# Kernel tuning notes

Measured on AMD Instinct MI355X. Metric: run time of the kernel, lower is better.

## Reference

```python
import jax, jax.numpy as jnp
import numpy as np

# tag2index constants
PAD, START, END, T = 0, 14, 15, 16
B, L, V, E, H = 128, 512, 30000, 256, 256


def _lstm(xs, w_ih, w_hh, b, reverse=False):
    """xs: [L, B, E] -> hs: [L, B, H]. PyTorch gate order i,f,g,o."""
    Bsz = xs.shape[1]
    Hd = w_hh.shape[1]
    def cell(carry, xt):
        h, c = carry
        g = xt @ w_ih.T + h @ w_hh.T + b  # [B, 4H]
        i, f, gg, o = jnp.split(g, 4, axis=-1)
        c = jax.nn.sigmoid(f) * c + jax.nn.sigmoid(i) * jnp.tanh(gg)
        h = jax.nn.sigmoid(o) * jnp.tanh(c)
        return (h, c), h
    init = (jnp.zeros((Bsz, Hd), xs.dtype), jnp.zeros((Bsz, Hd), xs.dtype))
    _, hs = jax.lax.scan(cell, init, xs, reverse=reverse)
    return hs


def setup_inputs() -> dict:
    key = jax.random.key(0)
    ks = jax.random.split(key, 12)
    batch_data = jax.random.randint(ks[0], (B, L), 0, V, dtype=jnp.int32)
    # variable-length tags with contiguous trailing PAD (as the model assumes)
    lengths = jax.random.randint(ks[1], (B,), L // 4, L + 1)
    raw_tags = jax.random.randint(ks[2], (B, L), 1, 14, dtype=jnp.int32)  # real tags in [1,14)
    pos = jnp.arange(L)[None, :]
    batch_tag = jnp.where(pos < lengths[:, None], raw_tags, PAD).astype(jnp.int32)
    s = 0.05
    emb = jax.random.normal(ks[3], (V, E), jnp.float32) * s
    w_ih_f = jax.random.normal(ks[4], (4 * H, E), jnp.float32) * s
    w_hh_f = jax.random.normal(ks[5], (4 * H, H), jnp.float32) * s
    b_f = jnp.zeros((4 * H,), jnp.float32)
    w_ih_b = jax.random.normal(ks[6], (4 * H, E), jnp.float32) * s
    w_hh_b = jax.random.normal(ks[7], (4 * H, H), jnp.float32) * s
    b_b = jnp.zeros((4 * H,), jnp.float32)
    w_cls = jax.random.normal(ks[8], (T, 2 * H), jnp.float32) * s
    b_cls = jnp.zeros((T,), jnp.float32)
    transition = jnp.full((T, T), 1.0 / T, jnp.float32)
    return {"batch_data": batch_data, "batch_tag": batch_tag, "emb": emb,
            "w_ih_f": w_ih_f, "w_hh_f": w_hh_f, "b_f": b_f,
            "w_ih_b": w_ih_b, "w_hh_b": w_hh_b, "b_b": b_b,
            "w_cls": w_cls, "b_cls": b_cls, "transition": transition}


def reference(batch_data, batch_tag, emb, w_ih_f, w_hh_f, b_f,
              w_ih_b, w_hh_b, b_b, w_cls, b_cls, transition):
    # ---- BiLSTM encoder ----
    x = emb[batch_data]                      # [B, L, E]
    xs = jnp.moveaxis(x, 1, 0)               # [L, B, E]
    hf = _lstm(xs, w_ih_f, w_hh_f, b_f, reverse=False)
    hb = _lstm(xs, w_ih_b, w_hh_b, b_b, reverse=True)
    out = jnp.moveaxis(jnp.concatenate([hf, hb], axis=-1), 0, 1)  # [B, L, 2H]
    emission = out @ w_cls.T + b_cls          # [B, L, T]
    crf_scores = emission[:, :, None, :] + transition[None, None]  # [B, L, T, T]

    # ---- CRF loss (linear-chain forward algorithm) ----
    mask = batch_tag != PAD                   # [B, L]
    lengths = mask.sum(axis=1)                # [B]
    prev = jnp.concatenate(
        [jnp.full((B, 1), START, batch_tag.dtype), batch_tag[:, :-1]], axis=1)
    idx = (batch_tag + prev * T).astype(jnp.int32)  # flat (prev_tag, cur_tag) index
    flat = crf_scores.reshape(B, L, T * T)
    g = jnp.take_along_axis(flat, idx[:, :, None], axis=2)[..., 0]
    golden_scores = jnp.sum(jnp.where(mask, g, 0.0))

    sc_t = jnp.moveaxis(crf_scores, 1, 0)     # [L, B, T, T]
    init = sc_t[0, :, START, :]               # [B, T] (all lengths >= 1)
    def step(prev_scores, x_t):
        sc, t = x_t
        new = jax.nn.logsumexp(sc + prev_scores[:, :, None], axis=1)  # [B, T]
        active = (lengths > t)[:, None]
        return jnp.where(active, new, prev_scores), None
    final, _ = jax.lax.scan(step, init, (sc_t[1:], jnp.arange(1, L)))
    all_path_scores = jnp.sum(final[:, END])
    loss = (all_path_scores - golden_scores) / B
    return loss
```

## Files before the change

kernel.cpp:

```cpp
#include <hip/hip_runtime.h>

#define Bsz 128
#define Lseq 512
#define Hdim 256
#define Tn 16
#define START_TAG 14
#define END_TAG 15

typedef float f32x4 __attribute__((ext_vector_type(4)));
typedef short s16x8 __attribute__((ext_vector_type(8)));

__device__ __forceinline__ unsigned short f2bf(float f) {
    unsigned int u = __builtin_bit_cast(unsigned int, f);
    u += 0x7fffu + ((u >> 16) & 1u);
    return (unsigned short)(u >> 16);
}
__device__ __forceinline__ float bf2f(unsigned int bits16) {
    return __builtin_bit_cast(float, bits16 << 16);
}
__device__ __forceinline__ float sigmoidf_(float x) {
    return 1.0f / (1.0f + __expf(-x));
}

__global__ void embprep_kernel(const float* __restrict__ emb,
                               unsigned int* __restrict__ embb, int n2) {
    int i = blockIdx.x * blockDim.x + threadIdx.x;
    int stride = gridDim.x * blockDim.x;
    for (; i < n2; i += stride)
        embb[i] = (unsigned int)f2bf(emb[2 * i]) | ((unsigned int)f2bf(emb[2 * i + 1]) << 16);
}

__global__ void wprep_kernel(const float* __restrict__ wih_f, const float* __restrict__ whh_f,
                             const float* __restrict__ wih_b, const float* __restrict__ whh_b,
                             unsigned int* __restrict__ wtile) {
    int bid = blockIdx.x;
    int ki  = bid & 15;
    int tl  = (bid >> 4) & 3;
    int ug  = (bid >> 6) & 15;
    int dir = bid >> 10;
    int t = threadIdx.x;
    int lane = t >> 2, j = t & 3;
    int n = lane & 15, kq = lane >> 4;
    int k0 = ki * 32 + kq * 8 + 2 * j;
    int col = tl * 256 + ug * 16 + n;
    const float* wih = dir ? wih_b : wih_f;
    const float* whh = dir ? whh_b : whh_f;
    float f0, f1;
    if (k0 < 256) { f0 = wih[col * 256 + k0];       f1 = wih[col * 256 + k0 + 1]; }
    else          { f0 = whh[col * 256 + k0 - 256]; f1 = whh[col * 256 + k0 - 255]; }
    wtile[(size_t)bid * 256 + t] = (unsigned int)f2bf(f0) | ((unsigned int)f2bf(f1) << 16);
}

__global__ void lengths_kernel(const int* __restrict__ tag, int* __restrict__ lengths) {
    int b = blockIdx.x;
    int tid = threadIdx.x;
    int cnt = 0;
    for (int l = tid; l < Lseq; l += blockDim.x)
        cnt += (tag[b * Lseq + l] != 0) ? 1 : 0;
    for (int off = 32; off > 0; off >>= 1) cnt += __shfl_down(cnt, off);
    __shared__ int red[4];
    if ((tid & 63) == 0) red[tid >> 6] = cnt;
    __syncthreads();
    if (tid == 0) lengths[b] = red[0] + red[1] + red[2] + red[3];
}

__global__ __launch_bounds__(256, 1) void bilstm_persist(
    const int* __restrict__ bd,
    const unsigned int* __restrict__ embb,
    const unsigned int* __restrict__ wtile,
    const float* __restrict__ b_f, const float* __restrict__ b_b,
    const float* __restrict__ w_cls,
    float* __restrict__ em_f, float* __restrict__ em_b,
    unsigned long long* __restrict__ ring)
{
    const int wg  = blockIdx.x;
    const int dir = wg >> 7;
    const int bg  = (wg >> 4) & 7;
    const int ug  = wg & 15;
    const int tid = threadIdx.x;
    const int gb0 = bg * 16;

    __shared__ unsigned int w_lds[16384];
    __shared__ unsigned int h_lds[16 * 132];
    __shared__ float g_lds[4][16][17];
    __shared__ float part_lds[16][17];
    __shared__ float bias_lds[64];
    __shared__ float wcls_lds[256];

    {
        const unsigned int* wsrc = wtile + ((size_t)(dir * 16 + ug) << 14);
        for (int i = 0; i < 16; ++i) {
            int idx = tid + 256 * i;
            uint4 v4 = *(const uint4*)(wsrc + (size_t)idx * 4);
            *(uint4*)&w_lds[idx * 4] = v4;
        }
        if (tid < 64) {
            const float* bias = dir ? b_b : b_f;
            bias_lds[tid] = bias[(tid >> 4) * 256 + ug * 16 + (tid & 15)];
        }
        wcls_lds[tid] = w_cls[(size_t)ug * (2 * Hdim) + dir * Hdim + tid];
        for (int i = tid; i < 16 * 132; i += 256) h_lds[i] = 0;
    }

    const int wv = tid >> 6;
    const int l  = tid & 63;
    const int n  = l & 15;
    const int kq = l >> 4;
    const int cb = tid >> 4, cu = tid & 15;
    const int em_m = tid >> 4, em_seg = tid & 15;
    const int hm = tid >> 4, hj0 = (tid & 15) * 8;
    float c_reg = 0.f;
    float* emout = dir ? em_b : em_f;
    const int* bd_row = bd + (size_t)(gb0 + n) * Lseq;

    unsigned long long* rbase = ring + (size_t)dir * 2 * 16384;

    __syncthreads();

    f32x4 acc_x = {0.f, 0.f, 0.f, 0.f};
    {
        const int t0 = dir ? (Lseq - 1) : 0;
        int tok = bd_row[t0];
        const unsigned int* xsrc = embb + (size_t)tok * 128 + kq * 4;
        #pragma unroll
        for (int ki = 0; ki < 8; ++ki) {
            uint4 xv = *(const uint4*)(xsrc + ki * 16);
            s16x8 a = __builtin_bit_cast(s16x8, xv);
            s16x8 b = *(const s16x8*)&w_lds[((wv * 16 + ki) * 64 + l) * 4];
            acc_x = __builtin_amdgcn_mfma_f32_16x16x32_bf16(a, b, acc_x, 0, 0, 0);
        }
    }
    int tok_next = (Lseq > 1) ? bd_row[dir ? (Lseq - 2) : 1] : 0;

    unsigned long long v[8];

    for (int s = 0; s < Lseq; ++s) {
        if (s > 0) {
            #pragma unroll
            for (int j = 0; j < 8; ++j)
                h_lds[hm * 132 + hj0 + j] = (unsigned int)v[j];
        }
        __syncthreads();

        if (s > 0) {
            const unsigned int* hr = &h_lds[em_m * 132 + em_seg * 8];
            const float* wc = &wcls_lds[em_seg * 16];
            float p = 0.f;
            #pragma unroll
            for (int j = 0; j < 8; ++j) {
                unsigned int w = hr[j];
                p += bf2f(w & 0xffffu) * wc[2 * j] + bf2f(w >> 16) * wc[2 * j + 1];
            }
            part_lds[em_m][em_seg] = p;
        }
        {
            f32x4 acc = acc_x;
            #pragma unroll
            for (int kih = 0; kih < 8; ++kih) {
                s16x8 a = *(const s16x8*)&h_lds[n * 132 + kih * 16 + kq * 4];
                s16x8 b = *(const s16x8*)&w_lds[(((wv * 16) + 8 + kih) * 64 + l) * 4];
                acc = __builtin_amdgcn_mfma_f32_16x16x32_bf16(a, b, acc, 0, 0, 0);
            }
            #pragma unroll
            for (int r = 0; r < 4; ++r)
                g_lds[wv][kq * 4 + r][n] = acc[r];
        }
        __syncthreads();

        {
            float gi = g_lds[0][cb][cu] + bias_lds[cu];
            float gf = g_lds[1][cb][cu] + bias_lds[16 + cu];
            float gg = g_lds[2][cb][cu] + bias_lds[32 + cu];
            float go = g_lds[3][cb][cu] + bias_lds[48 + cu];
            float cn = sigmoidf_(gf) * c_reg + sigmoidf_(gi) * tanhf(gg);
            c_reg = cn;
            float hn = sigmoidf_(go) * tanhf(cn);
            unsigned int hbits = (unsigned int)f2bf(hn);
            unsigned int other = (unsigned int)__shfl_down((int)hbits, 1);
            if ((cu & 1) == 0) {
                unsigned long long pk = (unsigned long long)(hbits | (other << 16))
                                      | ((unsigned long long)(s + 1) << 32);
                __hip_atomic_store(
                    rbase + ((size_t)(s & 1) * 16384) + (size_t)(gb0 + cb) * 128 + ug * 8 + (cu >> 1),
                    pk, __ATOMIC_RELAXED, __HIP_MEMORY_SCOPE_AGENT);
            }
        }

        if (s + 1 < Lseq) {
            const unsigned int* xsrc = embb + (size_t)tok_next * 128 + kq * 4;
            f32x4 ax = {0.f, 0.f, 0.f, 0.f};
            #pragma unroll
            for (int ki = 0; ki < 8; ++ki) {
                uint4 xv = *(const uint4*)(xsrc + ki * 16);
                s16x8 a = __builtin_bit_cast(s16x8, xv);
                s16x8 b = *(const s16x8*)&w_lds[((wv * 16 + ki) * 64 + l) * 4];
                ax = __builtin_amdgcn_mfma_f32_16x16x32_bf16(a, b, ax, 0, 0, 0);
            }
            acc_x = ax;
        }
        if (s + 2 < Lseq)
            tok_next = bd_row[dir ? (Lseq - 3 - s) : (s + 2)];

        const unsigned long long* src =
            rbase + ((size_t)(s & 1) * 16384) + (size_t)(gb0 + hm) * 128 + hj0;
        #pragma unroll
        for (int j = 0; j < 8; ++j)
            v[j] = __hip_atomic_load(src + j, __ATOMIC_RELAXED, __HIP_MEMORY_SCOPE_AGENT);

        if (s > 0 && tid < 16) {
            float ssum = 0.f;
            #pragma unroll
            for (int q = 0; q < 16; ++q) ssum += part_lds[tid][q];
            int t_prev = dir ? (Lseq - s) : (s - 1);
            emout[((size_t)(gb0 + tid) * Lseq + t_prev) * Tn + ug] = ssum;
        }

        {
            const unsigned long long want = (unsigned long long)(s + 1);
            unsigned int pend = 0xffu;
            int tries = 0;
            while (true) {
                #pragma unroll
                for (int j = 0; j < 8; ++j)
                    if ((pend & (1u << j)) && ((v[j] >> 32) == want))
                        pend &= ~(1u << j);
                if (!pend) break;
                if (tries++ > 0) __builtin_amdgcn_s_sleep(2);
                #pragma unroll
                for (int j = 0; j < 8; ++j)
                    if (pend & (1u << j))
                        v[j] = __hip_atomic_load(src + j, __ATOMIC_RELAXED,
                                                 __HIP_MEMORY_SCOPE_AGENT);
            }
        }
    }

    {
        #pragma unroll
        for (int j = 0; j < 8; ++j)
            h_lds[hm * 132 + hj0 + j] = (unsigned int)v[j];
        __syncthreads();
        {
            const unsigned int* hr = &h_lds[em_m * 132 + em_seg * 8];
            const float* wc = &wcls_lds[em_seg * 16];
            float p = 0.f;
            #pragma unroll
            for (int j = 0; j < 8; ++j) {
                unsigned int vv = hr[j];
                p += bf2f(vv & 0xffffu) * wc[2 * j] + bf2f(vv >> 16) * wc[2 * j + 1];
            }
            part_lds[em_m][em_seg] = p;
        }
        __syncthreads();
        if (tid < 16) {
            float ssum = 0.f;
            #pragma unroll
            for (int q = 0; q < 16; ++q) ssum += part_lds[tid][q];
            int t_tail = dir ? 0 : (Lseq - 1);
            emout[((size_t)(gb0 + tid) * Lseq + t_tail) * Tn + ug] = ssum;
        }
    }
}

__global__ void golden_kernel(const int* __restrict__ tag,
                              const float* __restrict__ em_f,
                              const float* __restrict__ em_b,
                              const float* __restrict__ b_cls,
                              const float* __restrict__ trans,
                              float* __restrict__ golden)
{
    int b = blockIdx.x;
    int tid = threadIdx.x;
    float s = 0.f;
    for (int l = tid; l < Lseq; l += blockDim.x) {
        int tg = tag[b * Lseq + l];
        if (tg != 0) {
            int prev = (l == 0) ? START_TAG : tag[b * Lseq + l - 1];
            size_t e = ((size_t)b * Lseq + l) * Tn + tg;
            s += em_f[e] + em_b[e] + b_cls[tg] + trans[prev * Tn + tg];
        }
    }
    for (int off = 32; off > 0; off >>= 1) s += __shfl_down(s, off);
    __shared__ float red[4];
    if ((tid & 63) == 0) red[tid >> 6] = s;
    __syncthreads();
    if (tid == 0) atomicAdd(golden, red[0] + red[1] + red[2] + red[3]);
}

__global__ void crf_forward_kernel(const float* __restrict__ em_f,
                                   const float* __restrict__ em_b,
                                   const float* __restrict__ b_cls,
                                   const float* __restrict__ trans,
                                   const int* __restrict__ lengths,
                                   float* __restrict__ allpath)
{
    int b = blockIdx.x;
    int lane = threadIdx.x;
    __shared__ float ems[Lseq * Tn];

    {
        const f32x4* pf = (const f32x4*)(em_f + (size_t)b * Lseq * Tn);
        const f32x4* pb = (const f32x4*)(em_b + (size_t)b * Lseq * Tn);
        f32x4* pd = (f32x4*)ems;
        for (int i = lane; i < Lseq * Tn / 4; i += 64) {
            f32x4 a = pf[i], c = pb[i];
            pd[i] = (f32x4){a[0] + c[0], a[1] + c[1], a[2] + c[2], a[3] + c[3]};
        }
    }
    __syncthreads();

    int j = lane & 15;
    float tcol[16];
    #pragma unroll
    for (int i = 0; i < 16; ++i) tcol[i] = trans[i * Tn + j];
    float bc = b_cls[j];
    float alpha = ems[j] + bc + tcol[START_TAG];
    int len = lengths[b];
    for (int t = 1; t < Lseq; ++t) {
        float av[16];
        float m = -1e30f;
        #pragma unroll
        for (int i = 0; i < 16; ++i) {
            av[i] = __shfl(alpha, i) + tcol[i];
            m = fmaxf(m, av[i]);
        }
        float sum = 0.f;
        #pragma unroll
        for (int i = 0; i < 16; ++i) sum += __expf(av[i] - m);
        float nv = ems[t * Tn + j] + bc + m + __logf(sum);
        alpha = (t < len) ? nv : alpha;
    }
    if (lane == END_TAG) atomicAdd(allpath, alpha);
}

__global__ void finalize_kernel(const float* __restrict__ scal, float* __restrict__ out) {
    out[0] = (scal[1] - scal[0]) / (float)Bsz;
}

extern "C" void kernel_launch(void* const* d_in, const int* in_sizes, int n_in,
                              void* d_out, int out_size, void* d_ws, size_t ws_size,
                              hipStream_t stream)
{
    (void)in_sizes; (void)n_in; (void)out_size; (void)ws_size;
    const int*   bd     = (const int*)d_in[0];
    const int*   tag    = (const int*)d_in[1];
    const float* emb    = (const float*)d_in[2];
    const float* w_ih_f = (const float*)d_in[3];
    const float* w_hh_f = (const float*)d_in[4];
    const float* b_f    = (const float*)d_in[5];
    const float* w_ih_b = (const float*)d_in[6];
    const float* w_hh_b = (const float*)d_in[7];
    const float* b_b    = (const float*)d_in[8];
    const float* w_cls  = (const float*)d_in[9];
    const float* b_cls  = (const float*)d_in[10];
    const float* trans  = (const float*)d_in[11];
    float* out = (float*)d_out;

    float* ws = (float*)d_ws;
    float* em_f = ws;
    float* em_b = em_f + (size_t)Bsz * Lseq * Tn;
    unsigned long long* ring =
        (unsigned long long*)(em_b + (size_t)Bsz * Lseq * Tn);
    float* scal = (float*)(ring + 65536);
    int* lengths = (int*)(scal + 8);
    unsigned int* wtile = (unsigned int*)(lengths + 128);
    unsigned int* embb = wtile + (size_t)524288;

    hipMemsetAsync(ring, 0, 65536 * 8 + 8 * sizeof(float), stream);

    embprep_kernel<<<2048, 256, 0, stream>>>(emb, embb, 30000 * 128);
    wprep_kernel<<<2048, 256, 0, stream>>>(w_ih_f, w_hh_f, w_ih_b, w_hh_b, wtile);
    lengths_kernel<<<Bsz, 256, 0, stream>>>(tag, lengths);

    void* kargs[] = {
        (void*)&bd, (void*)&embb, (void*)&wtile,
        (void*)&b_f, (void*)&b_b, (void*)&w_cls,
        (void*)&em_f, (void*)&em_b,
        (void*)&ring
    };
    hipLaunchCooperativeKernel((const void*)bilstm_persist,
                               dim3(256), dim3(256), kargs, 0, stream);

    golden_kernel<<<Bsz, 256, 0, stream>>>(tag, em_f, em_b, b_cls, trans, scal);
    crf_forward_kernel<<<Bsz, 64, 0, stream>>>(em_f, em_b, b_cls, trans, lengths, scal + 1);
    finalize_kernel<<<1, 1, 0, stream>>>(scal, out);
}
```

Baseline: 2.181 ms.

## Split batch tile into two half-groups to overlap recurrence exchange with compute

The 16-row batch tile in each workgroup is split into two 8-row subgroups that alternate half-steps. While one half's hidden state is exchanged through the global ring buffer, the other half's gate MFMA and cell update run, which is meant to hide cross-workgroup sync latency. Embedding loads are issued into registers ahead of the barrier. __syncthreads is replaced with a barrier that waits only on LDS counters, so outstanding global loads are not drained at each barrier. The cost is twice as many loop iterations and barriers, and each MFMA still computes all 16 rows while only half are used per half-step.

```diff
diff --git a/kernel.cpp b/kernel.cpp
--- a/kernel.cpp
+++ b/kernel.cpp
@@ -20,6 +20,14 @@
 }
 __device__ __forceinline__ float sigmoidf_(float x) {
     return 1.0f / (1.0f + __expf(-x));
+}
+
+__device__ __forceinline__ void wg_barrier_lds() {
+    __builtin_amdgcn_sched_barrier(0);
+    asm volatile("s_waitcnt lgkmcnt(0)" ::: "memory");
+    __builtin_amdgcn_sched_barrier(0);
+    __builtin_amdgcn_s_barrier();
+    __builtin_amdgcn_sched_barrier(0);
 }
 
 __global__ void embprep_kernel(const float* __restrict__ emb,
@@ -107,54 +115,85 @@
     const int n  = l & 15;
     const int kq = l >> 4;
     const int cb = tid >> 4, cu = tid & 15;
-    const int em_m = tid >> 4, em_seg = tid & 15;
-    const int hm = tid >> 4, hj0 = (tid & 15) * 8;
+    const int rrow = tid >> 5;
+    const int rw0  = (tid & 31) * 4;
     float c_reg = 0.f;
     float* emout = dir ? em_b : em_f;
-    const int* bd_row = bd + (size_t)(gb0 + n) * Lseq;
 
     unsigned long long* rbase = ring + (size_t)dir * 2 * 16384;
 
     __syncthreads();
 
-    f32x4 acc_x = {0.f, 0.f, 0.f, 0.f};
+    f32x4 acc_xA = {0.f, 0.f, 0.f, 0.f};
+    f32x4 acc_xB = {0.f, 0.f, 0.f, 0.f};
     {
         const int t0 = dir ? (Lseq - 1) : 0;
-        int tok = bd_row[t0];
-        const unsigned int* xsrc = embb + (size_t)tok * 128 + kq * 4;
+        int tokA = bd[(size_t)(gb0 + (n & 7)) * Lseq + t0];
+        int tokB = bd[(size_t)(gb0 + 8 + (n & 7)) * Lseq + t0];
+        const unsigned int* xa = embb + (size_t)tokA * 128 + kq * 4;
+        const unsigned int* xb = embb + (size_t)tokB * 128 + kq * 4;
         #pragma unroll
         for (int ki = 0; ki < 8; ++ki) {
-            uint4 xv = *(const uint4*)(xsrc + ki * 16);
-            s16x8 a = __builtin_bit_cast(s16x8, xv);
             s16x8 b = *(const s16x8*)&w_lds[((wv * 16 + ki) * 64 + l) * 4];
-            acc_x = __builtin_amdgcn_mfma_f32_16x16x32_bf16(a, b, acc_x, 0, 0, 0);
-        }
-    }
-    int tok_next = (Lseq > 1) ? bd_row[dir ? (Lseq - 2) : 1] : 0;
-
-    unsigned long long v[8];
-
-    for (int s = 0; s < Lseq; ++s) {
+            s16x8 aA = __builtin_bit_cast(s16x8, *(const uint4*)(xa + ki * 16));
+            acc_xA = __builtin_amdgcn_mfma_f32_16x16x32_bf16(aA, b, acc_xA, 0, 0, 0);
+            s16x8 aB = __builtin_bit_cast(s16x8, *(const uint4*)(xb + ki * 16));
+            acc_xB = __builtin_amdgcn_mfma_f32_16x16x32_bf16(aB, b, acc_xB, 0, 0, 0);
+        }
+    }
+    const int t1 = dir ? (Lseq - 2) : 1;
+    int tokA_next = (Lseq > 1) ? bd[(size_t)(gb0 + (n & 7)) * Lseq + t1] : 0;
+    int tokB_next = (Lseq > 1) ? bd[(size_t)(gb0 + 8 + (n & 7)) * Lseq + t1] : 0;
+
+    unsigned long long v[4];
+
+    for (int i = 0; i < 2 * Lseq; ++i) {
+        const int sg = i & 1;
+        const int s  = i >> 1;
+
         if (s > 0) {
-            #pragma unroll
-            for (int j = 0; j < 8; ++j)
-                h_lds[hm * 132 + hj0 + j] = (unsigned int)v[j];
-        }
-        __syncthreads();
-
-        if (s > 0) {
-            const unsigned int* hr = &h_lds[em_m * 132 + em_seg * 8];
-            const float* wc = &wcls_lds[em_seg * 16];
+            int row = sg * 8 + rrow;
+            #pragma unroll
+            for (int j = 0; j < 4; ++j)
+                h_lds[row * 132 + rw0 + j] = (unsigned int)v[j];
+        }
+
+        const unsigned long long* psrc = nullptr;
+        if (i >= 1) {
+            const int ps = (i - 1) >> 1;
+            psrc = rbase + (size_t)(ps & 1) * 16384
+                 + (size_t)(gb0 + (sg ^ 1) * 8 + rrow) * 128 + rw0;
+            #pragma unroll
+            for (int j = 0; j < 4; ++j)
+                v[j] = __hip_atomic_load(psrc + j, __ATOMIC_RELAXED, __HIP_MEMORY_SCOPE_AGENT);
+        }
+
+        uint4 xg[8];
+        const bool do_x = (s + 1 < Lseq);
+        if (do_x) {
+            int tok = sg ? tokB_next : tokA_next;
+            const unsigned int* xsrc = embb + (size_t)tok * 128 + kq * 4;
+            #pragma unroll
+            for (int ki = 0; ki < 8; ++ki)
+                xg[ki] = *(const uint4*)(xsrc + ki * 16);
+        }
+
+        wg_barrier_lds();
+
+        if (s > 0 && tid < 128) {
+            int m_loc = tid >> 4, seg = tid & 15;
+            const unsigned int* hr = &h_lds[(sg * 8 + m_loc) * 132 + seg * 8];
+            const float* wc = &wcls_lds[seg * 16];
             float p = 0.f;
             #pragma unroll
             for (int j = 0; j < 8; ++j) {
                 unsigned int w = hr[j];
                 p += bf2f(w & 0xffffu) * wc[2 * j] + bf2f(w >> 16) * wc[2 * j + 1];
             }
-            part_lds[em_m][em_seg] = p;
+            part_lds[m_loc][seg] = p;
         }
         {
-            f32x4 acc = acc_x;
+            f32x4 acc = sg ? acc_xB : acc_xA;
             #pragma unroll
             for (int kih = 0; kih < 8; ++kih) {
                 s16x8 a = *(const s16x8*)&h_lds[n * 132 + kih * 16 + kq * 4];
@@ -165,9 +204,10 @@
             for (int r = 0; r < 4; ++r)
                 g_lds[wv][kq * 4 + r][n] = acc[r];
         }
-        __syncthreads();
-
-        {
+
+        wg_barrier_lds();
+
+        if ((cb >> 3) == sg) {
             float gi = g_lds[0][cb][cu] + bias_lds[cu];
             float gf = g_lds[1][cb][cu] + bias_lds[16 + cu];
             float gg = g_lds[2][cb][cu] + bias_lds[32 + cu];
@@ -186,50 +226,45 @@
             }
         }
 
-        if (s + 1 < Lseq) {
-            const unsigned int* xsrc = embb + (size_t)tok_next * 128 + kq * 4;
+        if (s > 0 && tid < 8) {
+            float ssum = 0.f;
+            #pragma unroll
+            for (int q = 0; q < 16; ++q) ssum += part_lds[tid][q];
+            int t_prev = dir ? (Lseq - s) : (s - 1);
+            emout[((size_t)(gb0 + sg * 8 + tid) * Lseq + t_prev) * Tn + ug] = ssum;
+        }
+
+        if (do_x) {
             f32x4 ax = {0.f, 0.f, 0.f, 0.f};
             #pragma unroll
             for (int ki = 0; ki < 8; ++ki) {
-                uint4 xv = *(const uint4*)(xsrc + ki * 16);
-                s16x8 a = __builtin_bit_cast(s16x8, xv);
+                s16x8 a = __builtin_bit_cast(s16x8, xg[ki]);
                 s16x8 b = *(const s16x8*)&w_lds[((wv * 16 + ki) * 64 + l) * 4];
                 ax = __builtin_amdgcn_mfma_f32_16x16x32_bf16(a, b, ax, 0, 0, 0);
             }
-            acc_x = ax;
-        }
-        if (s + 2 < Lseq)
-            tok_next = bd_row[dir ? (Lseq - 3 - s) : (s + 2)];
-
-        const unsigned long long* src =
-            rbase + ((size_t)(s & 1) * 16384) + (size_t)(gb0 + hm) * 128 + hj0;
-        #pragma unroll
-        for (int j = 0; j < 8; ++j)
-            v[j] = __hip_atomic_load(src + j, __ATOMIC_RELAXED, __HIP_MEMORY_SCOPE_AGENT);
-
-        if (s > 0 && tid < 16) {
-            float ssum = 0.f;
-            #pragma unroll
-            for (int q = 0; q < 16; ++q) ssum += part_lds[tid][q];
-            int t_prev = dir ? (Lseq - s) : (s - 1);
-            emout[((size_t)(gb0 + tid) * Lseq + t_prev) * Tn + ug] = ssum;
-        }
-
-        {
-            const unsigned long long want = (unsigned long long)(s + 1);
-            unsigned int pend = 0xffu;
+            if (sg) acc_xB = ax; else acc_xA = ax;
+        }
+        if (s + 2 < Lseq) {
+            int t2 = dir ? (Lseq - 3 - s) : (s + 2);
+            int tok2 = bd[(size_t)(gb0 + sg * 8 + (n & 7)) * Lseq + t2];
+            if (sg) tokB_next = tok2; else tokA_next = tok2;
+        }
+
+        if (i >= 1) {
+            const unsigned long long want = (unsigned long long)(((i - 1) >> 1) + 1);
+            unsigned int pend = 0xfu;
             int tries = 0;
             while (true) {
                 #pragma unroll
-                for (int j = 0; j < 8; ++j)
+                for (int j = 0; j < 4; ++j)
                     if ((pend & (1u << j)) && ((v[j] >> 32) == want))
                         pend &= ~(1u << j);
                 if (!pend) break;
                 if (tries++ > 0) __builtin_amdgcn_s_sleep(2);
                 #pragma unroll
-                for (int j = 0; j < 8; ++j)
+                for (int j = 0; j < 4; ++j)
                     if (pend & (1u << j))
-                        v[j] = __hip_atomic_load(src + j, __ATOMIC_RELAXED,
+                        v[j] = __hip_atomic_load(psrc + j, __ATOMIC_RELAXED,
                                                  __HIP_MEMORY_SCOPE_AGENT);
             }
         }
@@ -237,10 +272,38 @@
 
     {
         #pragma unroll
-        for (int j = 0; j < 8; ++j)
-            h_lds[hm * 132 + hj0 + j] = (unsigned int)v[j];
+        for (int j = 0; j < 4; ++j)
+            h_lds[rrow * 132 + rw0 + j] = (unsigned int)v[j];
+        const unsigned long long* psrc = rbase + (size_t)16384
+            + (size_t)(gb0 + 8 + rrow) * 128 + rw0;
+        unsigned long long w[4];
+        const unsigned long long want = 512ull;
+        #pragma unroll
+        for (int j = 0; j < 4; ++j)
+            w[j] = __hip_atomic_load(psrc + j, __ATOMIC_RELAXED, __HIP_MEMORY_SCOPE_AGENT);
+        {
+            unsigned int pend = 0xfu;
+            int tries = 0;
+            while (true) {
+                #pragma unroll
+                for (int j = 0; j < 4; ++j)
+                    if ((pend & (1u << j)) && ((w[j] >> 32) == want))
+                        pend &= ~(1u << j);
+                if (!pend) break;
+                if (tries++ > 0) __builtin_amdgcn_s_sleep(2);
+                #pragma unroll
+                for (int j = 0; j < 4; ++j)
+                    if (pend & (1u << j))
+                        w[j] = __hip_atomic_load(psrc + j, __ATOMIC_RELAXED,
+                                                 __HIP_MEMORY_SCOPE_AGENT);
+            }
+        }
+        #pragma unroll
+        for (int j = 0; j < 4; ++j)
+            h_lds[(8 + rrow) * 132 + rw0 + j] = (unsigned int)w[j];
         __syncthreads();
         {
+            const int em_m = tid >> 4, em_seg = tid & 15;
             const unsigned int* hr = &h_lds[em_m * 132 + em_seg * 8];
             const float* wc = &wcls_lds[em_seg * 16];
             float p = 0.f;
```

Result: slower. 2.701 ms (+23.9%).
